# Optimization experiments

Measured on AMD Instinct MI355X. Metric: run time of the kernel, lower is better.

Reference implementation:

```python
import jax, jax.numpy as jnp
import numpy as np

N = 100000
E = 1600000
D_IN = 128
F = 128


def _glorot(key, shape, scale=1.0):
    fan_in, fan_out = shape
    std = jnp.sqrt(2.0 / (fan_in + fan_out))
    return jax.random.normal(key, shape, dtype=jnp.float32) * std * scale


def setup_inputs() -> dict:
    key = jax.random.key(0)
    ks = jax.random.split(key, 10)
    h = jax.random.normal(ks[0], (N, D_IN), dtype=jnp.float32)
    # ensure every node appears as a row (src) so degree >= 1 (no inf in deg**-0.5)
    src_extra = jax.random.randint(ks[1], (E - N,), 0, N, dtype=jnp.int32)
    edge_src = jnp.concatenate([jnp.arange(N, dtype=jnp.int32), src_extra])
    edge_dst = jax.random.randint(ks[2], (E,), 0, N, dtype=jnp.int32)
    # faithful to original: fake indices sampled in [0, E) (jnp indexing clamps)
    src_fake = jax.random.randint(ks[3], (E,), 0, E, dtype=jnp.int32)
    dst_fake = jax.random.randint(ks[4], (E,), 0, E, dtype=jnp.int32)
    w_gcn0 = _glorot(ks[5], (D_IN, F))
    w_gcn1 = _glorot(ks[6], (F, F))
    # small scale on rate0 head to keep exp(sum over F dims) finite in fp32
    w_rate0 = _glorot(ks[7], (F, F), scale=0.05)
    w_rate1 = _glorot(ks[8], (F, 1))
    w_alpha = _glorot(ks[9], (F, 1))
    return {"h": h, "w_gcn0": w_gcn0, "w_gcn1": w_gcn1, "w_rate0": w_rate0,
            "w_rate1": w_rate1, "w_alpha": w_alpha, "edge_src": edge_src,
            "edge_dst": edge_dst, "src_fake": src_fake, "dst_fake": dst_fake}


def _gcn(h, W, norm, edge_src, edge_dst):
    h = h * norm                     # [N, d] degree pre-norm
    h = h @ W                        # dense projection
    h = jax.ops.segment_sum(h[edge_dst], edge_src, num_segments=N)  # a @ h
    return h * norm                  # degree post-norm


def reference(h, w_gcn0, w_gcn1, w_rate0, w_rate1, w_alpha,
              edge_src, edge_dst, src_fake, dst_fake):
    ones = jnp.ones((E,), dtype=h.dtype)
    deg = jax.ops.segment_sum(ones, edge_src, num_segments=N)  # row sums of a
    norm = (deg ** -0.5)[:, None]

    h = _gcn(h, w_gcn0, norm, edge_src, edge_dst)
    h = _gcn(h, w_gcn1, norm, edge_src, edge_dst)

    rate0 = h @ w_rate0   # [N, F]
    rate1 = h @ w_rate1   # [N, 1]
    alpha = h @ w_alpha   # [N, 1]

    src, dst = edge_src, edge_dst
    rate0_real = jnp.exp((rate0[src] + rate0[dst]).sum(-1))
    rate1_real = jnp.exp((rate1[src] + rate1[dst]).sum(-1))
    alpha_real = jax.nn.sigmoid((alpha[src] * alpha[dst]).sum(-1) / alpha.shape[-1] ** 0.5)

    # faithful to original (including rate0+rate1 mix and /shape (not sqrt) in alpha_fake)
    rate0_fake = jnp.exp((rate0[src_fake] + rate1[dst_fake]).sum(-1))
    rate1_fake = jnp.exp((rate1[src_fake] + rate1[dst_fake]).sum(-1))
    alpha_fake = jax.nn.sigmoid((alpha[src] * alpha[dst_fake]).sum(-1) / alpha.shape[-1])

    return jnp.stack([rate0_real, rate1_real, alpha_real,
                      rate0_fake, rate1_fake, alpha_fake])  # [6, E]
```

## Files before the change

### kernel.cpp

```cpp
#include <hip/hip_runtime.h>
#include <math.h>

#define NN 100000
#define EE 1600000
#define KB 256
#define RR 391
#define CAP 8192
#define PARTB 782
#define PROJB 391


__global__ __launch_bounds__(256) void k_init(int* __restrict__ gcur) {
    gcur[threadIdx.x] = 0;
}


__global__ __launch_bounds__(256) void k_part_pmat(const int* __restrict__ src, const int* __restrict__ dst,
                                                   int* __restrict__ gcur, unsigned int* __restrict__ pk,
                                                   const float* __restrict__ w_gcn0,
                                                   const float* __restrict__ w_gcn1,
                                                   const float* __restrict__ w_rate0,
                                                   const float* __restrict__ w_rate1,
                                                   const float* __restrict__ w_alpha,
                                                   float* __restrict__ Pt0, float* __restrict__ Pt1,
                                                   float* __restrict__ Pt2) {
    int t = threadIdx.x;
    if (blockIdx.x < PARTB) {
        __shared__ int cnt[KB];
        __shared__ int base[KB];
        cnt[t] = 0;
        __syncthreads();
        int e0 = blockIdx.x * 2048 + t * 8;
        unsigned int pkv[8];
        int bkt[8];
        if (e0 + 8 <= EE) {
            int4 sa = *(const int4*)(src + e0);
            int4 sb = *(const int4*)(src + e0 + 4);
            int4 da = *(const int4*)(dst + e0);
            int4 db = *(const int4*)(dst + e0 + 4);
            int ss[8] = { sa.x, sa.y, sa.z, sa.w, sb.x, sb.y, sb.z, sb.w };
            int dd[8] = { da.x, da.y, da.z, da.w, db.x, db.y, db.z, db.w };
            #pragma unroll
            for (int i = 0; i < 8; ++i) {
                int b = ss[i] / RR;
                bkt[i] = b;
                pkv[i] = (unsigned int)dd[i] | ((unsigned int)(ss[i] - b * RR) << 17);
                atomicAdd(&cnt[b], 1);
            }
        } else {
            #pragma unroll
            for (int i = 0; i < 8; ++i) {
                int e = e0 + i;
                if (e < EE) {
                    int s = src[e], d = dst[e];
                    int b = s / RR;
                    bkt[i] = b;
                    pkv[i] = (unsigned int)d | ((unsigned int)(s - b * RR) << 17);
                    atomicAdd(&cnt[b], 1);
                } else bkt[i] = -1;
            }
        }
        __syncthreads();
        base[t] = cnt[t] ? atomicAdd(&gcur[t], cnt[t]) : 0;
        __syncthreads();
        cnt[t] = 0;
        __syncthreads();
        #pragma unroll
        for (int i = 0; i < 8; ++i) {
            if (bkt[i] >= 0) {
                int rr = atomicAdd(&cnt[bkt[i]], 1);
                int rel = base[bkt[i]] + rr;
                if (rel < CAP) pk[bkt[i] * CAP + rel] = pkv[i];
            }
        }
    } else {
        __shared__ float V0[128], V1[128], V2[128];
        __shared__ float Q0[128], Q1[128], Q2[128];
        int r = t >> 1, seg = t & 1;
        {
            const float4* p = (const float4*)(w_rate0 + r * 128 + seg * 64);
            float s = 0.f;
            #pragma unroll
            for (int k = 0; k < 16; ++k) { float4 v = p[k]; s += v.x + v.y + v.z + v.w; }
            s += __shfl_down(s, 1, 2);
            if (seg == 0) V0[r] = s;
        }
        if (t < 128) { V1[t] = w_rate1[t]; V2[t] = w_alpha[t]; }
        __syncthreads();
        {
            const float4* p = (const float4*)(w_gcn1 + r * 128 + seg * 64);
            float q0 = 0.f, q1 = 0.f, q2 = 0.f;
            #pragma unroll
            for (int k = 0; k < 16; ++k) {
                float4 w = p[k];
                int j = seg * 64 + k * 4;
                q0 += w.x * V0[j] + w.y * V0[j+1] + w.z * V0[j+2] + w.w * V0[j+3];
                q1 += w.x * V1[j] + w.y * V1[j+1] + w.z * V1[j+2] + w.w * V1[j+3];
                q2 += w.x * V2[j] + w.y * V2[j+1] + w.z * V2[j+2] + w.w * V2[j+3];
            }
            q0 += __shfl_down(q0, 1, 2);
            q1 += __shfl_down(q1, 1, 2);
            q2 += __shfl_down(q2, 1, 2);
            if (seg == 0) { Q0[r] = q0; Q1[r] = q1; Q2[r] = q2; }
        }
        __syncthreads();
        {
            const float4* p = (const float4*)(w_gcn0 + r * 128 + seg * 64);
            float q0 = 0.f, q1 = 0.f, q2 = 0.f;
            #pragma unroll
            for (int k = 0; k < 16; ++k) {
                float4 w = p[k];
                int j = seg * 64 + k * 4;
                q0 += w.x * Q0[j] + w.y * Q0[j+1] + w.z * Q0[j+2] + w.w * Q0[j+3];
                q1 += w.x * Q1[j] + w.y * Q1[j+1] + w.z * Q1[j+2] + w.w * Q1[j+3];
                q2 += w.x * Q2[j] + w.y * Q2[j+1] + w.z * Q2[j+2] + w.w * Q2[j+3];
            }
            q0 += __shfl_down(q0, 1, 2);
            q1 += __shfl_down(q1, 1, 2);
            q2 += __shfl_down(q2, 1, 2);
            if (seg == 0) { Pt0[r] = q0; Pt1[r] = q1; Pt2[r] = q2; }
        }
    }
}


__global__ __launch_bounds__(512) void k_proj_cnt(const unsigned int* __restrict__ pk,
                                                  const int* __restrict__ gcur,
                                                  const float* __restrict__ h,
                                                  const float* __restrict__ Pt0, const float* __restrict__ Pt1,
                                                  const float* __restrict__ Pt2,
                                                  float* __restrict__ nrm, float4* __restrict__ u4) {
    int t = threadIdx.x;
    if (blockIdx.x < PROJB) {
        __shared__ float sP0[128], sP1[128], sP2[128];
        if (t < 128) { sP0[t] = Pt0[t]; sP1[t] = Pt1[t]; sP2[t] = Pt2[t]; }
        __syncthreads();
        int hw = t >> 5;
        int l32 = t & 31;
        int c4 = l32 * 4;
        float4 c0 = *(const float4*)(sP0 + c4);
        float4 c1 = *(const float4*)(sP1 + c4);
        float4 c2 = *(const float4*)(sP2 + c4);
        int nlo = blockIdx.x * 256;
        for (int i0 = 0; i0 < 256; i0 += 16) {
            int node = nlo + i0 + hw;
            if (node < NN) {
                float4 hv = *(const float4*)(h + (size_t)node * 128 + c4);
                float p0v = hv.x * c0.x + hv.y * c0.y + hv.z * c0.z + hv.w * c0.w;
                float p1v = hv.x * c1.x + hv.y * c1.y + hv.z * c1.z + hv.w * c1.w;
                float p2v = hv.x * c2.x + hv.y * c2.y + hv.z * c2.z + hv.w * c2.w;
                #pragma unroll
                for (int off = 16; off > 0; off >>= 1) {
                    p0v += __shfl_down(p0v, off, 32);
                    p1v += __shfl_down(p1v, off, 32);
                    p2v += __shfl_down(p2v, off, 32);
                }
                if (l32 == 0) {
                    float* up = (float*)&u4[node];
                    *(float2*)up = make_float2(p0v, p1v);
                    up[2] = p2v;
                }
            }
        }
    } else {
        __shared__ int c[RR];
        int b = blockIdx.x - PROJB;
        int nlo = b * RR;
        int nn = NN - nlo; if (nn > RR) nn = RR;
        if (nn <= 0) return;
        if (t < RR) c[t] = 0;
        __syncthreads();
        const unsigned int* P = pk + b * CAP;
        int m = gcur[b]; if (m > CAP) m = CAP;
        for (int i = t; i < m; i += 512) atomicAdd(&c[P[i] >> 17], 1);
        __syncthreads();
        if (t < nn) {
            float nv = rsqrtf((float)c[t]);
            nrm[nlo + t] = nv;
            ((float*)&u4[nlo + t])[3] = nv;
        }
    }
}


template<int MODE>
__global__ __launch_bounds__(1024) void k_agg(const unsigned int* __restrict__ pk,
                                              const int* __restrict__ gcur,
                                              const float4* __restrict__ T, const float* __restrict__ nrm,
                                              float4* __restrict__ outv) {
    __shared__ float s0[RR], s1[RR], s2[RR];
    int b = blockIdx.x;
    int t = threadIdx.x;
    int nlo = b * RR;
    int nn = NN - nlo; if (nn > RR) nn = RR;
    if (nn <= 0) return;
    if (t < RR) { s0[t] = 0.f; s1[t] = 0.f; s2[t] = 0.f; }
    __syncthreads();
    const unsigned int* P = pk + b * CAP;
    int m = gcur[b]; if (m > CAP) m = CAP;
    int i = t;
    for (; i + 1024 < m; i += 2048) {
        unsigned int wa = P[i];
        unsigned int wb = P[i + 1024];
        float4 va = T[wa & 0x1FFFFu];
        float4 vb = T[wb & 0x1FFFFu];
        float ax = va.x, ay = va.y, az = va.z;
        float bx = vb.x, by = vb.y, bz = vb.z;
        if (MODE == 1) { ax *= va.w; ay *= va.w; az *= va.w; bx *= vb.w; by *= vb.w; bz *= vb.w; }
        int ra = (int)(wa >> 17), rb = (int)(wb >> 17);
        atomicAdd(&s0[ra], ax); atomicAdd(&s1[ra], ay); atomicAdd(&s2[ra], az);
        atomicAdd(&s0[rb], bx); atomicAdd(&s1[rb], by); atomicAdd(&s2[rb], bz);
    }
    if (i < m) {
        unsigned int wa = P[i];
        float4 va = T[wa & 0x1FFFFu];
        float ax = va.x, ay = va.y, az = va.z;
        if (MODE == 1) { ax *= va.w; ay *= va.w; az *= va.w; }
        int ra = (int)(wa >> 17);
        atomicAdd(&s0[ra], ax); atomicAdd(&s1[ra], ay); atomicAdd(&s2[ra], az);
    }
    __syncthreads();
    for (int j = t; j < nn; j += 1024) {
        float nv = nrm[nlo + j];
        float sc = (MODE == 1) ? nv * nv : nv;
        outv[nlo + j] = make_float4(sc * s0[j], sc * s1[j], sc * s2[j], 0.f);
    }
}


__global__ __launch_bounds__(256) void k_edge(const int* __restrict__ esrc, const int* __restrict__ edst,
                                              const int* __restrict__ sfake, const int* __restrict__ dfake,
                                              const float4* __restrict__ p4, float* __restrict__ out) {
    int t = threadIdx.x;
    int e0 = blockIdx.x * 1024 + t * 4;
    if (e0 >= EE) return;
    int4 s4  = *(const int4*)(esrc + e0);
    int4 d4  = *(const int4*)(edst + e0);
    int4 sf4 = *(const int4*)(sfake + e0);
    int4 df4 = *(const int4*)(dfake + e0);
    int ss[4] = { s4.x, s4.y, s4.z, s4.w };
    int dd[4] = { d4.x, d4.y, d4.z, d4.w };
    int sf[4] = { sf4.x, sf4.y, sf4.z, sf4.w };
    int df[4] = { df4.x, df4.y, df4.z, df4.w };
    float o0[4], o1[4], o2[4], o3[4], o4[4], o5[4];
    #pragma unroll
    for (int j = 0; j < 4; ++j) {
        int sfj = sf[j]; sfj = sfj < 0 ? 0 : (sfj >= NN ? NN - 1 : sfj);
        int dfj = df[j]; dfj = dfj < 0 ? 0 : (dfj >= NN ? NN - 1 : dfj);
        float4 ps = p4[ss[j]], pd = p4[dd[j]], psf = p4[sfj], pdf = p4[dfj];
        o0[j] = expf(ps.x + pd.x);
        o1[j] = expf(ps.y + pd.y);
        o2[j] = 1.f / (1.f + expf(-(ps.z * pd.z)));
        o3[j] = expf(psf.x + 128.f * pdf.y);
        o4[j] = expf(psf.y + pdf.y);
        o5[j] = 1.f / (1.f + expf(-(ps.z * pdf.z)));
    }
    *(float4*)(out + e0)                  = make_float4(o0[0], o0[1], o0[2], o0[3]);
    *(float4*)(out + (size_t)EE + e0)     = make_float4(o1[0], o1[1], o1[2], o1[3]);
    *(float4*)(out + (size_t)2 * EE + e0) = make_float4(o2[0], o2[1], o2[2], o2[3]);
    *(float4*)(out + (size_t)3 * EE + e0) = make_float4(o3[0], o3[1], o3[2], o3[3]);
    *(float4*)(out + (size_t)4 * EE + e0) = make_float4(o4[0], o4[1], o4[2], o4[3]);
    *(float4*)(out + (size_t)5 * EE + e0) = make_float4(o5[0], o5[1], o5[2], o5[3]);
}


extern "C" void kernel_launch(void* const* d_in, const int* in_sizes, int n_in,
                              void* d_out, int out_size, void* d_ws, size_t ws_size,
                              hipStream_t stream) {
    const float* h       = (const float*)d_in[0];
    const float* w_gcn0  = (const float*)d_in[1];
    const float* w_gcn1  = (const float*)d_in[2];
    const float* w_rate0 = (const float*)d_in[3];
    const float* w_rate1 = (const float*)d_in[4];
    const float* w_alpha = (const float*)d_in[5];
    const int* edge_src  = (const int*)d_in[6];
    const int* edge_dst  = (const int*)d_in[7];
    const int* src_fake  = (const int*)d_in[8];
    const int* dst_fake  = (const int*)d_in[9];
    float* out = (float*)d_out;

    char* p = (char*)d_ws;
    auto alloc = [&](size_t bytes) {
        char* r = p;
        p += (bytes + 255) & ~(size_t)255;
        return r;
    };
    unsigned int* pk = (unsigned int*)alloc((size_t)KB * CAP * 4);
    int* gcur   = (int*)alloc(KB * 4);
    float* nrm  = (float*)alloc((size_t)NN * 4);
    float4* u4  = (float4*)alloc((size_t)NN * 16);
    float4* z4  = (float4*)alloc((size_t)NN * 16);
    float4* p4  = (float4*)alloc((size_t)NN * 16);
    float* Pt0  = (float*)alloc(512);
    float* Pt1  = (float*)alloc(512);
    float* Pt2  = (float*)alloc(512);

    k_init<<<1, KB, 0, stream>>>(gcur);
    k_part_pmat<<<PARTB + 1, 256, 0, stream>>>(edge_src, edge_dst, gcur, pk,
                                               w_gcn0, w_gcn1, w_rate0, w_rate1, w_alpha,
                                               Pt0, Pt1, Pt2);
    k_proj_cnt<<<PROJB + KB, 512, 0, stream>>>(pk, gcur, h, Pt0, Pt1, Pt2, nrm, u4);
    k_agg<1><<<KB, 1024, 0, stream>>>(pk, gcur, u4, nrm, z4);
    k_agg<2><<<KB, 1024, 0, stream>>>(pk, gcur, z4, nrm, p4);
    k_edge<<<(EE + 1023) / 1024, 256, 0, stream>>>(edge_src, edge_dst, src_fake, dst_fake, p4, out);
}
```

Baseline: 239.0 us.

## Fuse edge partitioning with node projection and recompute weight vectors per block

Edge bucketing and the node feature projection now run in one kernel with interleaved block roles. Each projection block recomputes the collapsed weight vectors itself, removing the dependency on a separate weight-collapse pass. Degree counting moves to its own kernel with 1024 threads. The aggregation loop is unrolled to four outstanding gathers per thread. The cost is redundant weight math in 391 blocks and higher shared-memory use per block.

```diff
diff --git a/kernel.cpp b/kernel.cpp
--- a/kernel.cpp
+++ b/kernel.cpp
@@ -6,8 +6,7 @@
 #define KB 256
 #define RR 391
 #define CAP 8192
-#define PARTB 782
-#define PROJB 391
+#define NPART 391
 
 
 __global__ __launch_bounds__(256) void k_init(int* __restrict__ gcur) {
@@ -15,22 +14,28 @@
 }
 
 
-__global__ __launch_bounds__(256) void k_part_pmat(const int* __restrict__ src, const int* __restrict__ dst,
+__global__ __launch_bounds__(512) void k_part_proj(const int* __restrict__ src, const int* __restrict__ dst,
                                                    int* __restrict__ gcur, unsigned int* __restrict__ pk,
+                                                   const float* __restrict__ h,
                                                    const float* __restrict__ w_gcn0,
                                                    const float* __restrict__ w_gcn1,
                                                    const float* __restrict__ w_rate0,
                                                    const float* __restrict__ w_rate1,
                                                    const float* __restrict__ w_alpha,
-                                                   float* __restrict__ Pt0, float* __restrict__ Pt1,
-                                                   float* __restrict__ Pt2) {
+                                                   float4* __restrict__ u4) {
+    __shared__ int cnt[KB];
+    __shared__ int base[KB];
+    __shared__ float V0[128], V1[128], V2[128];
+    __shared__ float Q0[128], Q1[128], Q2[128];
+    __shared__ alignas(16) float sP0[128], sP1[128], sP2[128];
     int t = threadIdx.x;
-    if (blockIdx.x < PARTB) {
-        __shared__ int cnt[KB];
-        __shared__ int base[KB];
-        cnt[t] = 0;
-        __syncthreads();
-        int e0 = blockIdx.x * 2048 + t * 8;
+    int role = blockIdx.x & 1;
+    int id = blockIdx.x >> 1;
+
+    if (role == 0) {
+        if (t < KB) cnt[t] = 0;
+        __syncthreads();
+        int e0 = id * 4096 + t * 8;
         unsigned int pkv[8];
         int bkt[8];
         if (e0 + 8 <= EE) {
@@ -61,9 +66,9 @@
             }
         }
         __syncthreads();
-        base[t] = cnt[t] ? atomicAdd(&gcur[t], cnt[t]) : 0;
-        __syncthreads();
-        cnt[t] = 0;
+        if (t < KB) base[t] = cnt[t] ? atomicAdd(&gcur[t], cnt[t]) : 0;
+        __syncthreads();
+        if (t < KB) cnt[t] = 0;
         __syncthreads();
         #pragma unroll
         for (int i = 0; i < 8; ++i) {
@@ -74,66 +79,50 @@
             }
         }
     } else {
-        __shared__ float V0[128], V1[128], V2[128];
-        __shared__ float Q0[128], Q1[128], Q2[128];
-        int r = t >> 1, seg = t & 1;
+        int r = t >> 2, seg = t & 3;
         {
-            const float4* p = (const float4*)(w_rate0 + r * 128 + seg * 64);
+            const float4* pp = (const float4*)(w_rate0 + r * 128 + seg * 32);
             float s = 0.f;
             #pragma unroll
-            for (int k = 0; k < 16; ++k) { float4 v = p[k]; s += v.x + v.y + v.z + v.w; }
-            s += __shfl_down(s, 1, 2);
+            for (int k = 0; k < 8; ++k) { float4 v = pp[k]; s += v.x + v.y + v.z + v.w; }
+            s += __shfl_down(s, 2, 4); s += __shfl_down(s, 1, 4);
             if (seg == 0) V0[r] = s;
         }
         if (t < 128) { V1[t] = w_rate1[t]; V2[t] = w_alpha[t]; }
         __syncthreads();
         {
-            const float4* p = (const float4*)(w_gcn1 + r * 128 + seg * 64);
+            const float4* pp = (const float4*)(w_gcn1 + r * 128 + seg * 32);
             float q0 = 0.f, q1 = 0.f, q2 = 0.f;
             #pragma unroll
-            for (int k = 0; k < 16; ++k) {
-                float4 w = p[k];
-                int j = seg * 64 + k * 4;
+            for (int k = 0; k < 8; ++k) {
+                float4 w = pp[k];
+                int j = seg * 32 + k * 4;
                 q0 += w.x * V0[j] + w.y * V0[j+1] + w.z * V0[j+2] + w.w * V0[j+3];
                 q1 += w.x * V1[j] + w.y * V1[j+1] + w.z * V1[j+2] + w.w * V1[j+3];
                 q2 += w.x * V2[j] + w.y * V2[j+1] + w.z * V2[j+2] + w.w * V2[j+3];
             }
-            q0 += __shfl_down(q0, 1, 2);
-            q1 += __shfl_down(q1, 1, 2);
-            q2 += __shfl_down(q2, 1, 2);
+            q0 += __shfl_down(q0, 2, 4); q0 += __shfl_down(q0, 1, 4);
+            q1 += __shfl_down(q1, 2, 4); q1 += __shfl_down(q1, 1, 4);
+            q2 += __shfl_down(q2, 2, 4); q2 += __shfl_down(q2, 1, 4);
             if (seg == 0) { Q0[r] = q0; Q1[r] = q1; Q2[r] = q2; }
         }
         __syncthreads();
         {
-            const float4* p = (const float4*)(w_gcn0 + r * 128 + seg * 64);
+            const float4* pp = (const float4*)(w_gcn0 + r * 128 + seg * 32);
             float q0 = 0.f, q1 = 0.f, q2 = 0.f;
             #pragma unroll
-            for (int k = 0; k < 16; ++k) {
-                float4 w = p[k];
-                int j = seg * 64 + k * 4;
+            for (int k = 0; k < 8; ++k) {
+                float4 w = pp[k];
+                int j = seg * 32 + k * 4;
                 q0 += w.x * Q0[j] + w.y * Q0[j+1] + w.z * Q0[j+2] + w.w * Q0[j+3];
                 q1 += w.x * Q1[j] + w.y * Q1[j+1] + w.z * Q1[j+2] + w.w * Q1[j+3];
                 q2 += w.x * Q2[j] + w.y * Q2[j+1] + w.z * Q2[j+2] + w.w * Q2[j+3];
             }
-            q0 += __shfl_down(q0, 1, 2);
-            q1 += __shfl_down(q1, 1, 2);
-            q2 += __shfl_down(q2, 1, 2);
-            if (seg == 0) { Pt0[r] = q0; Pt1[r] = q1; Pt2[r] = q2; }
-        }
-    }
-}
-
-
-__global__ __launch_bounds__(512) void k_proj_cnt(const unsigned int* __restrict__ pk,
-                                                  const int* __restrict__ gcur,
-                                                  const float* __restrict__ h,
-                                                  const float* __restrict__ Pt0, const float* __restrict__ Pt1,
-                                                  const float* __restrict__ Pt2,
-                                                  float* __restrict__ nrm, float4* __restrict__ u4) {
-    int t = threadIdx.x;
-    if (blockIdx.x < PROJB) {
-        __shared__ float sP0[128], sP1[128], sP2[128];
-        if (t < 128) { sP0[t] = Pt0[t]; sP1[t] = Pt1[t]; sP2[t] = Pt2[t]; }
+            q0 += __shfl_down(q0, 2, 4); q0 += __shfl_down(q0, 1, 4);
+            q1 += __shfl_down(q1, 2, 4); q1 += __shfl_down(q1, 1, 4);
+            q2 += __shfl_down(q2, 2, 4); q2 += __shfl_down(q2, 1, 4);
+            if (seg == 0) { sP0[r] = q0; sP1[r] = q1; sP2[r] = q2; }
+        }
         __syncthreads();
         int hw = t >> 5;
         int l32 = t & 31;
@@ -141,7 +130,7 @@
         float4 c0 = *(const float4*)(sP0 + c4);
         float4 c1 = *(const float4*)(sP1 + c4);
         float4 c2 = *(const float4*)(sP2 + c4);
-        int nlo = blockIdx.x * 256;
+        int nlo = id * 256;
         for (int i0 = 0; i0 < 256; i0 += 16) {
             int node = nlo + i0 + hw;
             if (node < NN) {
@@ -162,23 +151,29 @@
                 }
             }
         }
-    } else {
-        __shared__ int c[RR];
-        int b = blockIdx.x - PROJB;
-        int nlo = b * RR;
-        int nn = NN - nlo; if (nn > RR) nn = RR;
-        if (nn <= 0) return;
-        if (t < RR) c[t] = 0;
-        __syncthreads();
-        const unsigned int* P = pk + b * CAP;
-        int m = gcur[b]; if (m > CAP) m = CAP;
-        for (int i = t; i < m; i += 512) atomicAdd(&c[P[i] >> 17], 1);
-        __syncthreads();
-        if (t < nn) {
-            float nv = rsqrtf((float)c[t]);
-            nrm[nlo + t] = nv;
-            ((float*)&u4[nlo + t])[3] = nv;
-        }
+    }
+}
+
+
+__global__ __launch_bounds__(1024) void k_cnt(const unsigned int* __restrict__ pk,
+                                              const int* __restrict__ gcur,
+                                              float* __restrict__ nrm, float4* __restrict__ u4) {
+    __shared__ int c[RR];
+    int b = blockIdx.x;
+    int t = threadIdx.x;
+    int nlo = b * RR;
+    int nn = NN - nlo; if (nn > RR) nn = RR;
+    if (nn <= 0) return;
+    if (t < RR) c[t] = 0;
+    __syncthreads();
+    const unsigned int* P = pk + b * CAP;
+    int m = gcur[b]; if (m > CAP) m = CAP;
+    for (int i = t; i < m; i += 1024) atomicAdd(&c[P[i] >> 17], 1);
+    __syncthreads();
+    if (t < nn) {
+        float nv = rsqrtf((float)c[t]);
+        nrm[nlo + t] = nv;
+        ((float*)&u4[nlo + t])[3] = nv;
     }
 }
 
@@ -199,19 +194,28 @@
     const unsigned int* P = pk + b * CAP;
     int m = gcur[b]; if (m > CAP) m = CAP;
     int i = t;
-    for (; i + 1024 < m; i += 2048) {
-        unsigned int wa = P[i];
-        unsigned int wb = P[i + 1024];
-        float4 va = T[wa & 0x1FFFFu];
-        float4 vb = T[wb & 0x1FFFFu];
-        float ax = va.x, ay = va.y, az = va.z;
-        float bx = vb.x, by = vb.y, bz = vb.z;
-        if (MODE == 1) { ax *= va.w; ay *= va.w; az *= va.w; bx *= vb.w; by *= vb.w; bz *= vb.w; }
-        int ra = (int)(wa >> 17), rb = (int)(wb >> 17);
-        atomicAdd(&s0[ra], ax); atomicAdd(&s1[ra], ay); atomicAdd(&s2[ra], az);
-        atomicAdd(&s0[rb], bx); atomicAdd(&s1[rb], by); atomicAdd(&s2[rb], bz);
-    }
-    if (i < m) {
+    for (; i + 3072 < m; i += 4096) {
+        unsigned int w0 = P[i];
+        unsigned int w1 = P[i + 1024];
+        unsigned int w2 = P[i + 2048];
+        unsigned int w3 = P[i + 3072];
+        float4 v0 = T[w0 & 0x1FFFFu];
+        float4 v1 = T[w1 & 0x1FFFFu];
+        float4 v2 = T[w2 & 0x1FFFFu];
+        float4 v3 = T[w3 & 0x1FFFFu];
+        if (MODE == 1) {
+            v0.x *= v0.w; v0.y *= v0.w; v0.z *= v0.w;
+            v1.x *= v1.w; v1.y *= v1.w; v1.z *= v1.w;
+            v2.x *= v2.w; v2.y *= v2.w; v2.z *= v2.w;
+            v3.x *= v3.w; v3.y *= v3.w; v3.z *= v3.w;
+        }
+        int r0 = (int)(w0 >> 17), r1 = (int)(w1 >> 17), r2 = (int)(w2 >> 17), r3 = (int)(w3 >> 17);
+        atomicAdd(&s0[r0], v0.x); atomicAdd(&s1[r0], v0.y); atomicAdd(&s2[r0], v0.z);
+        atomicAdd(&s0[r1], v1.x); atomicAdd(&s1[r1], v1.y); atomicAdd(&s2[r1], v1.z);
+        atomicAdd(&s0[r2], v2.x); atomicAdd(&s1[r2], v2.y); atomicAdd(&s2[r2], v2.z);
+        atomicAdd(&s0[r3], v3.x); atomicAdd(&s1[r3], v3.y); atomicAdd(&s2[r3], v3.z);
+    }
+    for (; i < m; i += 1024) {
         unsigned int wa = P[i];
         float4 va = T[wa & 0x1FFFFu];
         float ax = va.x, ay = va.y, az = va.z;
@@ -291,15 +295,11 @@
     float4* u4  = (float4*)alloc((size_t)NN * 16);
     float4* z4  = (float4*)alloc((size_t)NN * 16);
     float4* p4  = (float4*)alloc((size_t)NN * 16);
-    float* Pt0  = (float*)alloc(512);
-    float* Pt1  = (float*)alloc(512);
-    float* Pt2  = (float*)alloc(512);
 
     k_init<<<1, KB, 0, stream>>>(gcur);
-    k_part_pmat<<<PARTB + 1, 256, 0, stream>>>(edge_src, edge_dst, gcur, pk,
-                                               w_gcn0, w_gcn1, w_rate0, w_rate1, w_alpha,
-                                               Pt0, Pt1, Pt2);
-    k_proj_cnt<<<PROJB + KB, 512, 0, stream>>>(pk, gcur, h, Pt0, Pt1, Pt2, nrm, u4);
+    k_part_proj<<<2 * NPART, 512, 0, stream>>>(edge_src, edge_dst, gcur, pk, h,
+                                               w_gcn0, w_gcn1, w_rate0, w_rate1, w_alpha, u4);
+    k_cnt<<<KB, 1024, 0, stream>>>(pk, gcur, nrm, u4);
     k_agg<1><<<KB, 1024, 0, stream>>>(pk, gcur, u4, nrm, z4);
     k_agg<2><<<KB, 1024, 0, stream>>>(pk, gcur, z4, nrm, p4);
     k_edge<<<(EE + 1023) / 1024, 256, 0, stream>>>(edge_src, edge_dst, src_fake, dst_fake, p4, out);
```

Measured after the change: 247.0 us. 3.3% more time.
